# Kernel tuning notes

Measured on AMD Instinct MI355X. Metric: run time of the kernel, lower is better.

## Reference

```python
import jax, jax.numpy as jnp
import numpy as np

MAX_CLASSES = 10
LN_EPS = 1e-5


def _g_features(L):
    # L: (B, T, k) logits -> sorted G-matrix fingerprint (B, k*(k+1)//2)
    P = jax.nn.softmax(L, axis=-1)
    T = P.shape[1]
    k = P.shape[-1]
    G = jnp.einsum('btk,btl->bkl', P, P) / T  # (B, k, k)
    diag = jnp.diagonal(G, axis1=1, axis2=2)  # (B, k)
    diag_sorted = jnp.sort(diag, axis=-1)[:, ::-1]
    iu0, iu1 = np.triu_indices(k, 1)
    off = G[:, iu0, iu1]  # (B, k*(k-1)//2)
    off_sorted = jnp.sort(off, axis=-1)[:, ::-1]
    return jnp.concatenate([diag_sorted, off_sorted], axis=-1)


def setup_inputs() -> dict:
    key = jax.random.key(0)
    ks = list(range(2, MAX_CLASSES + 1))
    keys = jax.random.split(key, len(ks) + 3)
    B, T = 256, 4096
    inp = {}
    for i, k in enumerate(ks):
        inp[f'logits_k{k}'] = jax.random.normal(keys[i], (B, T, k), dtype=jnp.float32)
    input_dim = sum(k * (k + 1) // 2 for k in ks)  # 219
    hidden = 256
    out_dim = MAX_CLASSES - 1
    inp['ln_gamma'] = jnp.ones((input_dim,), jnp.float32)
    inp['ln_beta'] = jnp.zeros((input_dim,), jnp.float32)
    inp['w1'] = jax.random.normal(keys[-3], (input_dim, hidden), jnp.float32) * 0.05
    inp['b1'] = jnp.zeros((hidden,), jnp.float32)
    inp['w2'] = jax.random.normal(keys[-2], (hidden, hidden), jnp.float32) * 0.05
    inp['b2'] = jnp.zeros((hidden,), jnp.float32)
    inp['w3'] = jax.random.normal(keys[-1], (hidden, out_dim), jnp.float32) * 0.05
    inp['b3'] = jnp.zeros((out_dim,), jnp.float32)
    return inp


def reference(logits_k2, logits_k3, logits_k4, logits_k5, logits_k6,
              logits_k7, logits_k8, logits_k9, logits_k10,
              ln_gamma, ln_beta, w1, b1, w2, b2, w3, b3):
    all_logits = [logits_k2, logits_k3, logits_k4, logits_k5, logits_k6,
                  logits_k7, logits_k8, logits_k9, logits_k10]
    feats = jnp.concatenate([_g_features(L) for L in all_logits], axis=-1)  # (B, 219)
    # LayerNorm over last dim
    mu = jnp.mean(feats, axis=-1, keepdims=True)
    var = jnp.var(feats, axis=-1, keepdims=True)
    x = (feats - mu) * jax.lax.rsqrt(var + LN_EPS) * ln_gamma + ln_beta
    # MLP (exact GELU, matching torch nn.GELU default)
    h = jax.nn.gelu(x @ w1 + b1, approximate=False)
    h = jax.nn.gelu(h @ w2 + b2, approximate=False)
    return h @ w3 + b3  # (B, max_classes-1)
```

## Files before the change

kernel.cpp:

```cpp
#include <hip/hip_runtime.h>
#include <hip/hip_bf16.h>
#include <math.h>

#define BB 256
#define TT 4096

__constant__ int SEGF[10] = {0, 3, 9, 19, 34, 55, 83, 119, 164, 219};

template <int K>
__device__ __forceinline__ void g_accum(const float* __restrict__ L,
                                        float* __restrict__ gseg,
                                        float* __restrict__ part ) {
    constexpr int NACC = K * (K + 1) / 2;
    const int b = blockIdx.x;
    const int tid = threadIdx.x;

    float acc[NACC];
#pragma unroll
    for (int i = 0; i < NACC; ++i) acc[i] = 0.f;

    const float* Lb = L + (size_t)b * TT * K;

    for (int t = tid; t < TT; t += 256) {
        const float* p = Lb + (size_t)t * K;
        float v[K];
#pragma unroll
        for (int j = 0; j < K; ++j) v[j] = p[j];

        float m = v[0];
#pragma unroll
        for (int j = 1; j < K; ++j) m = fmaxf(m, v[j]);

        float s = 0.f;
#pragma unroll
        for (int j = 0; j < K; ++j) { v[j] = __expf(v[j] - m); s += v[j]; }
        const float inv = 1.0f / s;
#pragma unroll
        for (int j = 0; j < K; ++j) v[j] *= inv;

        int idx = 0;
#pragma unroll
        for (int i = 0; i < K; ++i) {
#pragma unroll
            for (int j = i; j < K; ++j) {
                acc[idx] = fmaf(v[i], v[j], acc[idx]);
                ++idx;
            }
        }
    }

    const int lane = tid & 63;
    const int wave = tid >> 6;
#pragma unroll
    for (int i = 0; i < NACC; ++i) {
        float x = acc[i];
#pragma unroll
        for (int off = 32; off > 0; off >>= 1) x += __shfl_down(x, off, 64);
        if (lane == 0) part[wave * 55 + i] = x;
    }
    __syncthreads();

    if (tid < NACC) {
        float x = part[0 * 55 + tid] + part[1 * 55 + tid] +
                  part[2 * 55 + tid] + part[3 * 55 + tid];
        x *= (1.0f / (float)TT);
        int i = 0, rem = tid;
        while (rem >= K - i) { rem -= K - i; ++i; }
        const int j = i + rem;
        int tgt;
        if (j == i) tgt = i;
        else tgt = K + i * (K - 1) - (i * (i - 1)) / 2 + (j - i - 1);
        gseg[tgt] = x;
    }
}

__global__ __launch_bounds__(256) void g_kernel(
    const float* __restrict__ l2, const float* __restrict__ l3,
    const float* __restrict__ l4, const float* __restrict__ l5,
    const float* __restrict__ l6, const float* __restrict__ l7,
    const float* __restrict__ l8, const float* __restrict__ l9,
    const float* __restrict__ l10, float* __restrict__ g) {
    __shared__ float part[4 * 55];
    float* gw = g + (size_t)blockIdx.x * 219;
    switch (blockIdx.y) {
        case 0: g_accum<2>(l2, gw + 0, part); break;
        case 1: g_accum<3>(l3, gw + 3, part); break;
        case 2: g_accum<4>(l4, gw + 9, part); break;
        case 3: g_accum<5>(l5, gw + 19, part); break;
        case 4: g_accum<6>(l6, gw + 34, part); break;
        case 5: g_accum<7>(l7, gw + 55, part); break;
        case 6: g_accum<8>(l8, gw + 83, part); break;
        case 7: g_accum<9>(l9, gw + 119, part); break;
        case 8: g_accum<10>(l10, gw + 164, part); break;
    }
}

__device__ __forceinline__ float gelu_exact(float x) {
    return 0.5f * x * (1.0f + erff(x * 0.70710678118654752440f));
}

__global__ __launch_bounds__(256) void head_kernel(
    const float* __restrict__ g, const float* __restrict__ gamma,
    const float* __restrict__ beta, const float* __restrict__ w1,
    const float* __restrict__ b1, const float* __restrict__ w2,
    const float* __restrict__ b2, const float* __restrict__ w3,
    const float* __restrict__ b3, float* __restrict__ out) {
    const int b = blockIdx.x;
    const int tid = threadIdx.x;

    __shared__ float pre[219];
    __shared__ float srt[219];
    __shared__ float xln[219];
    __shared__ float h1[256];
    __shared__ float h2[256];
    __shared__ float rs1[4], rs2[4];
    __shared__ float smu, srv;

    if (tid < 219) pre[tid] = g[(size_t)b * 219 + tid];
    __syncthreads();

    if (tid < 219) {
        int ik = 0;
        while (tid >= SEGF[ik + 1]) ++ik;
        const int K = ik + 2;
        const int base = SEGF[ik];
        const int local = tid - base;
        int sstart, slen, lidx;
        if (local < K) { sstart = base; slen = K; lidx = local; }
        else { sstart = base + K; slen = (K * (K - 1)) / 2; lidx = local - K; }
        const float v = pre[tid];
        int rank = 0;
        for (int m = 0; m < slen; ++m) {
            const float u = pre[sstart + m];
            rank += (u > v) || ((u == v) && (m < lidx));
        }
        srt[sstart + rank] = v;
    }
    __syncthreads();

    const float val = (tid < 219) ? srt[tid] : 0.f;
    float s1 = val, s2 = val * val;
#pragma unroll
    for (int off = 32; off > 0; off >>= 1) {
        s1 += __shfl_down(s1, off, 64);
        s2 += __shfl_down(s2, off, 64);
    }
    const int wave = tid >> 6, lane = tid & 63;
    if (lane == 0) { rs1[wave] = s1; rs2[wave] = s2; }
    __syncthreads();
    if (tid == 0) {
        const float t1 = rs1[0] + rs1[1] + rs1[2] + rs1[3];
        const float t2 = rs2[0] + rs2[1] + rs2[2] + rs2[3];
        const float mu = t1 * (1.0f / 219.0f);
        const float var = t2 * (1.0f / 219.0f) - mu * mu;
        smu = mu;
        srv = rsqrtf(var + 1e-5f);
    }
    __syncthreads();
    if (tid < 219) xln[tid] = (srt[tid] - smu) * srv * gamma[tid] + beta[tid];
    __syncthreads();

    {
        float a = b1[tid];
#pragma unroll 8
        for (int i = 0; i < 219; ++i) a = fmaf(xln[i], w1[i * 256 + tid], a);
        h1[tid] = gelu_exact(a);
    }
    __syncthreads();

    {
        float c = b2[tid];
#pragma unroll 8
        for (int i = 0; i < 256; ++i) c = fmaf(h1[i], w2[i * 256 + tid], c);
        h2[tid] = gelu_exact(c);
    }
    __syncthreads();

    if (tid < 9) {
        float o = b3[tid];
#pragma unroll 8
        for (int i = 0; i < 256; ++i) o = fmaf(h2[i], w3[i * 9 + tid], o);
        out[(size_t)b * 9 + tid] = o;
    }
}

extern "C" void kernel_launch(void* const* d_in, const int* in_sizes, int n_in,
                              void* d_out, int out_size, void* d_ws,
                              size_t ws_size, hipStream_t stream) {
    const float* l2 = (const float*)d_in[0];
    const float* l3 = (const float*)d_in[1];
    const float* l4 = (const float*)d_in[2];
    const float* l5 = (const float*)d_in[3];
    const float* l6 = (const float*)d_in[4];
    const float* l7 = (const float*)d_in[5];
    const float* l8 = (const float*)d_in[6];
    const float* l9 = (const float*)d_in[7];
    const float* l10 = (const float*)d_in[8];
    const float* gamma = (const float*)d_in[9];
    const float* beta = (const float*)d_in[10];
    const float* w1 = (const float*)d_in[11];
    const float* b1 = (const float*)d_in[12];
    const float* w2 = (const float*)d_in[13];
    const float* b2 = (const float*)d_in[14];
    const float* w3 = (const float*)d_in[15];
    const float* b3 = (const float*)d_in[16];

    float* gbuf = (float*)d_ws;
    float* outp = (float*)d_out;

    dim3 gridA(BB, 9);
    g_kernel<<<gridA, 256, 0, stream>>>(l2, l3, l4, l5, l6, l7, l8, l9, l10,
                                        gbuf);
    head_kernel<<<BB, 256, 0, stream>>>(gbuf, gamma, beta, w1, b1, w2, b2, w3,
                                        b3, outp);
}
```

Before: 84.57 us.

## Vectorize logits loads, split T into two chunks, schedule largest K first

The Gram-matrix kernel now gives each thread 4 consecutive timesteps and loads them as K float4 vectors instead of scalar strided loads. The T dimension is split across two blocks per (batch, k), so the grid grows from 2304 to 4608 blocks, and blocks for the largest K are scheduled first. The head kernel sums the two partial results and applies the 1/T scaling. This targets memory-bandwidth efficiency and load balance, at the cost of more register pressure for large K and a slightly larger workspace.

```diff
diff --git a/kernel.cpp b/kernel.cpp
--- a/kernel.cpp
+++ b/kernel.cpp
@@ -5,46 +5,57 @@
 #define BB 256
 #define TT 4096
 
+typedef float f4 __attribute__((ext_vector_type(4)));
+
 __constant__ int SEGF[10] = {0, 3, 9, 19, 34, 55, 83, 119, 164, 219};
 
 template <int K>
 __device__ __forceinline__ void g_accum(const float* __restrict__ L,
-                                        float* __restrict__ gseg,
-                                        float* __restrict__ part ) {
+                                        float* __restrict__ gdst,
+                                        float* __restrict__ part, int b,
+                                        int ch) {
     constexpr int NACC = K * (K + 1) / 2;
-    const int b = blockIdx.x;
     const int tid = threadIdx.x;
 
     float acc[NACC];
 #pragma unroll
     for (int i = 0; i < NACC; ++i) acc[i] = 0.f;
 
-    const float* Lb = L + (size_t)b * TT * K;
-
-    for (int t = tid; t < TT; t += 256) {
-        const float* p = Lb + (size_t)t * K;
-        float v[K];
-#pragma unroll
-        for (int j = 0; j < K; ++j) v[j] = p[j];
-
-        float m = v[0];
-#pragma unroll
-        for (int j = 1; j < K; ++j) m = fmaxf(m, v[j]);
-
-        float s = 0.f;
-#pragma unroll
-        for (int j = 0; j < K; ++j) { v[j] = __expf(v[j] - m); s += v[j]; }
-        const float inv = 1.0f / s;
-#pragma unroll
-        for (int j = 0; j < K; ++j) v[j] *= inv;
-
-        int idx = 0;
-#pragma unroll
-        for (int i = 0; i < K; ++i) {
-#pragma unroll
-            for (int j = i; j < K; ++j) {
-                acc[idx] = fmaf(v[i], v[j], acc[idx]);
-                ++idx;
+    const float* Lb = L + (size_t)b * TT * K + (size_t)ch * 2048 * K;
+
+#pragma unroll
+    for (int j = 0; j < 2; ++j) {
+        const int g = tid + j * 256;
+        const float* p = Lb + (size_t)g * 4 * K;
+        f4 q[K];
+#pragma unroll
+        for (int f = 0; f < K; ++f) q[f] = *(const f4*)(p + 4 * f);
+
+#pragma unroll
+        for (int r = 0; r < 4; ++r) {
+            float v[K];
+#pragma unroll
+            for (int c = 0; c < K; ++c) {
+                const int fl = r * K + c;
+                v[c] = q[fl >> 2][fl & 3];
+            }
+            float m = v[0];
+#pragma unroll
+            for (int c = 1; c < K; ++c) m = fmaxf(m, v[c]);
+            float s = 0.f;
+#pragma unroll
+            for (int c = 0; c < K; ++c) { v[c] = __expf(v[c] - m); s += v[c]; }
+            const float inv = 1.0f / s;
+#pragma unroll
+            for (int c = 0; c < K; ++c) v[c] *= inv;
+            int idx = 0;
+#pragma unroll
+            for (int i = 0; i < K; ++i) {
+#pragma unroll
+                for (int jj = i; jj < K; ++jj) {
+                    acc[idx] = fmaf(v[i], v[jj], acc[idx]);
+                    ++idx;
+                }
             }
         }
     }
@@ -61,16 +72,15 @@
     __syncthreads();
 
     if (tid < NACC) {
-        float x = part[0 * 55 + tid] + part[1 * 55 + tid] +
-                  part[2 * 55 + tid] + part[3 * 55 + tid];
-        x *= (1.0f / (float)TT);
+        const float x = part[0 * 55 + tid] + part[1 * 55 + tid] +
+                        part[2 * 55 + tid] + part[3 * 55 + tid];
         int i = 0, rem = tid;
         while (rem >= K - i) { rem -= K - i; ++i; }
         const int j = i + rem;
         int tgt;
         if (j == i) tgt = i;
         else tgt = K + i * (K - 1) - (i * (i - 1)) / 2 + (j - i - 1);
-        gseg[tgt] = x;
+        gdst[tgt] = x;
     }
 }
 
@@ -79,19 +89,25 @@
     const float* __restrict__ l4, const float* __restrict__ l5,
     const float* __restrict__ l6, const float* __restrict__ l7,
     const float* __restrict__ l8, const float* __restrict__ l9,
-    const float* __restrict__ l10, float* __restrict__ g) {
+    const float* __restrict__ l10, float* __restrict__ ws) {
     __shared__ float part[4 * 55];
-    float* gw = g + (size_t)blockIdx.x * 219;
-    switch (blockIdx.y) {
-        case 0: g_accum<2>(l2, gw + 0, part); break;
-        case 1: g_accum<3>(l3, gw + 3, part); break;
-        case 2: g_accum<4>(l4, gw + 9, part); break;
-        case 3: g_accum<5>(l5, gw + 19, part); break;
-        case 4: g_accum<6>(l6, gw + 34, part); break;
-        case 5: g_accum<7>(l7, gw + 55, part); break;
-        case 6: g_accum<8>(l8, gw + 83, part); break;
-        case 7: g_accum<9>(l9, gw + 119, part); break;
-        case 8: g_accum<10>(l10, gw + 164, part); break;
+    const int flat = blockIdx.x;
+    const int kslot = flat >> 9;
+    const int kidx = 8 - kslot;
+    const int idx = flat & 511;
+    const int b = idx >> 1;
+    const int ch = idx & 1;
+    float* gdst = ws + ((size_t)(b * 9 + kidx) * 2 + ch) * 55;
+    switch (kidx) {
+        case 0: g_accum<2>(l2, gdst, part, b, ch); break;
+        case 1: g_accum<3>(l3, gdst, part, b, ch); break;
+        case 2: g_accum<4>(l4, gdst, part, b, ch); break;
+        case 3: g_accum<5>(l5, gdst, part, b, ch); break;
+        case 4: g_accum<6>(l6, gdst, part, b, ch); break;
+        case 5: g_accum<7>(l7, gdst, part, b, ch); break;
+        case 6: g_accum<8>(l8, gdst, part, b, ch); break;
+        case 7: g_accum<9>(l9, gdst, part, b, ch); break;
+        case 8: g_accum<10>(l10, gdst, part, b, ch); break;
     }
 }
 
@@ -100,7 +116,7 @@
 }
 
 __global__ __launch_bounds__(256) void head_kernel(
-    const float* __restrict__ g, const float* __restrict__ gamma,
+    const float* __restrict__ ws, const float* __restrict__ gamma,
     const float* __restrict__ beta, const float* __restrict__ w1,
     const float* __restrict__ b1, const float* __restrict__ w2,
     const float* __restrict__ b2, const float* __restrict__ w3,
@@ -116,7 +132,13 @@
     __shared__ float rs1[4], rs2[4];
     __shared__ float smu, srv;
 
-    if (tid < 219) pre[tid] = g[(size_t)b * 219 + tid];
+    if (tid < 219) {
+        int ik = 0;
+        while (tid >= SEGF[ik + 1]) ++ik;
+        const int local = tid - SEGF[ik];
+        const float* p0 = ws + ((size_t)(b * 9 + ik) * 2) * 55;
+        pre[tid] = (p0[local] + p0[55 + local]) * (1.0f / (float)TT);
+    }
     __syncthreads();
 
     if (tid < 219) {
@@ -205,12 +227,11 @@
     const float* w3 = (const float*)d_in[15];
     const float* b3 = (const float*)d_in[16];
 
-    float* gbuf = (float*)d_ws;
+    float* wsf = (float*)d_ws;
     float* outp = (float*)d_out;
 
-    dim3 gridA(BB, 9);
-    g_kernel<<<gridA, 256, 0, stream>>>(l2, l3, l4, l5, l6, l7, l8, l9, l10,
-                                        gbuf);
-    head_kernel<<<BB, 256, 0, stream>>>(gbuf, gamma, beta, w1, b1, w2, b2, w3,
+    g_kernel<<<9 * 512, 256, 0, stream>>>(l2, l3, l4, l5, l6, l7, l8, l9, l10,
+                                          wsf);
+    head_kernel<<<BB, 256, 0, stream>>>(wsf, gamma, beta, w1, b1, w2, b2, w3,
                                         b3, outp);
 }
```

New measurement: 93.50 us. +10.6%, slower.
